# Optimization experiments

Measured on AMD Instinct MI355X. Metric: run time of the kernel, lower is better.

The kernel has to match this reference:

```python
import jax, jax.numpy as jnp
import numpy as np

NUM_USERS = 100000
NUM_BOOKS = 50000
HIDDEN = 128
USER_FEAT = 256
BOOK_FEAT = 256
E_PER_REL = 500000
NUM_LAYERS = 2


def setup_inputs() -> dict:
    key = jax.random.key(0)
    ks = jax.random.split(key, 10)
    user_x = jax.random.normal(ks[0], (NUM_USERS, USER_FEAT), dtype=jnp.float32)
    book_x = jax.random.normal(ks[1], (NUM_BOOKS, BOOK_FEAT), dtype=jnp.float32)
    user_W = jax.random.normal(ks[2], (HIDDEN, USER_FEAT), dtype=jnp.float32) * 0.05
    user_b = jax.random.normal(ks[3], (HIDDEN,), dtype=jnp.float32) * 0.05
    book_W = jax.random.normal(ks[4], (HIDDEN, BOOK_FEAT), dtype=jnp.float32) * 0.05
    book_b = jax.random.normal(ks[5], (HIDDEN,), dtype=jnp.float32) * 0.05
    # edge_index[0] = user indices, edge_index[1] = book indices
    rates_edge = jnp.stack([
        jax.random.randint(ks[6], (E_PER_REL,), 0, NUM_USERS),
        jax.random.randint(ks[7], (E_PER_REL,), 0, NUM_BOOKS)])
    implicit_edge = jnp.stack([
        jax.random.randint(ks[8], (E_PER_REL,), 0, NUM_USERS),
        jax.random.randint(ks[9], (E_PER_REL,), 0, NUM_BOOKS)])
    return {"user_x": user_x, "book_x": book_x, "user_W": user_W,
            "user_b": user_b, "book_W": book_W, "book_b": book_b,
            "rates_edge": rates_edge, "implicit_edge": implicit_edge}


def _lightgcn(user_x, book_x, user_W, user_b, book_W, book_b, rates_edge, implicit_edge):
    num_users = user_x.shape[0]
    num_nodes = num_users + book_x.shape[0]
    # input projections
    cu = user_x @ user_W.T + user_b  # [U, H]
    cb = book_x @ book_W.T + book_b  # [B, H]
    user_embeds = [cu]
    book_embeds = [cb]
    # build full directed edge list exactly as in the torch source
    all_edges = jnp.concatenate([rates_edge, implicit_edge], axis=1)  # [2, E]
    book_to_user = jnp.stack([all_edges[1] + num_users, all_edges[0]])
    full_edge = jnp.concatenate([all_edges, book_to_user], axis=1)  # [2, 2E]
    row, col = full_edge[0], full_edge[1]
    # symmetric degree normalization (edges fixed across layers)
    deg = jax.ops.segment_sum(jnp.ones(col.shape, dtype=cu.dtype), col,
                              num_segments=num_nodes)
    deg_inv_sqrt = jnp.where(deg > 0, jax.lax.rsqrt(jnp.maximum(deg, 1.0) * 0 + jnp.where(deg > 0, deg, 1.0)), 0.0)
    deg_inv_sqrt = jnp.where(deg > 0, jax.lax.rsqrt(jnp.where(deg > 0, deg, 1.0)), 0.0)
    norm = deg_inv_sqrt[row] * deg_inv_sqrt[col]  # [2E]
    for _ in range(NUM_LAYERS):
        x = jnp.concatenate([cu, cb], axis=0)  # [U+B, H]
        msg = x[row] * norm[:, None]           # gather + scale, [2E, H]
        out = jax.ops.segment_sum(msg, col, num_segments=num_nodes)  # scatter-add
        cu = out[:num_users]
        cb = out[num_users:]
        user_embeds.append(cu)
        book_embeds.append(cb)
    final_user = jnp.mean(jnp.stack(user_embeds), axis=0)
    final_book = jnp.mean(jnp.stack(book_embeds), axis=0)
    return final_user, final_book


def reference(user_x, book_x, user_W, user_b, book_W, book_b, rates_edge, implicit_edge):
    return _lightgcn(user_x, book_x, user_W, user_b, book_W, book_b,
                     rates_edge, implicit_edge)
```

## Files before the change

kernel.cpp:

```cpp
#include <hip/hip_runtime.h>

#define NUSERS 100000
#define NBOOKS 50000
#define HID 128
#define FEAT 256
#define EPR 500000
#define NEDGE (2 * EPR)

#define UBLK64 ((NUSERS + 63) / 64)
#define BBLK64 ((NBOOKS + 63) / 64)
#define GH_BLOCKS (UBLK64 + BBLK64)
#define FILL_B ((NEDGE + 255) / 256)
#define DIS_B ((NUSERS + 255) / 256)

typedef __attribute__((ext_vector_type(8))) short bf16x8;
typedef __attribute__((ext_vector_type(4))) float f32x4;

__device__ __forceinline__ unsigned short f2bf(float f) {
  union { float f; unsigned u; } v; v.f = f;
  unsigned r = v.u + 0x7FFFu + ((v.u >> 16) & 1u);
  return (unsigned short)(r >> 16);
}
__device__ __forceinline__ float bf2f(unsigned short h) {
  union { unsigned u; float f; } v; v.u = ((unsigned)h) << 16;
  return v.f;
}
__device__ __forceinline__ unsigned pk2bf(float lo, float hi) {
  unsigned r;
  asm("v_cvt_pk_bf16_f32 %0, %1, %2" : "=v"(r) : "v"(lo), "v"(hi));
  return r;
}

__global__ void cast_w(const float* __restrict__ w0, const float* __restrict__ w1,
                       unsigned short* __restrict__ o0, unsigned short* __restrict__ o1)
{
  int i = blockIdx.x * 256 + threadIdx.x;
  if (i < HID * FEAT) { o0[i] = f2bf(w0[i]); o1[i] = f2bf(w1[i]); }
}

__device__ __forceinline__ void decode_edge(const int* __restrict__ rates,
                                            const int* __restrict__ impl,
                                            int i, int& u, int& bk)
{
  if (i < EPR) { u = rates[i]; bk = rates[EPR + i]; }
  else { int j = i - EPR; u = impl[j]; bk = impl[EPR + j]; }
}

__global__ __launch_bounds__(256) void gemm_hist(
    const float* __restrict__ Xu, const float* __restrict__ Xb,
    const unsigned short* __restrict__ Wu, const unsigned short* __restrict__ Wb,
    const float* __restrict__ bu, const float* __restrict__ bb,
    unsigned short* __restrict__ cu0b, float* __restrict__ outb,
    float* __restrict__ outu,
    const int* __restrict__ rates, const int* __restrict__ impl,
    int* __restrict__ degu, int* __restrict__ cntb,
    int* __restrict__ relpos)
{
  __shared__ float Asb[64 * 256];
  const int bid = blockIdx.x;
  const int tid = threadIdx.x;

  const int e0 = bid * 512 + tid;
  const int e1 = e0 + 256;
  const bool v0 = e0 < NEDGE, v1 = e1 < NEDGE;
  int p0 = 0, p1 = 0;
  if (v0) {
    int u, bk;
    decode_edge(rates, impl, e0, u, bk);
    p0 = atomicAdd(&cntb[bk], 1);
    atomicAdd(&degu[u], 1);
  }
  if (v1) {
    int u, bk;
    decode_edge(rates, impl, e1, u, bk);
    p1 = atomicAdd(&cntb[bk], 1);
    atomicAdd(&degu[u], 1);
  }

  const bool isU = bid < UBLK64;
  const float* __restrict__ X = isU ? Xu : Xb;
  const unsigned short* __restrict__ W = isU ? Wu : Wb;
  const float* __restrict__ bias = isU ? bu : bb;
  const int M  = isU ? NUSERS : NBOOKS;
  const int bm = (isU ? bid : bid - UBLK64) * 64;

  const int lane = tid & 63;
  const int wv   = tid >> 6;
  const int l15  = lane & 15, l4 = lane >> 4;

#pragma unroll
  for (int rnd = 0; rnd < 16; ++rnd) {
    int o   = wv * 1024 + rnd * 64 + lane;
    int row = o >> 6;
    int pc  = o & 63;
    int lc  = pc ^ (row & 7);
    int gr  = bm + row; if (gr > M - 1) gr = M - 1;
    __builtin_amdgcn_global_load_lds(
        (const float*)&X[(size_t)gr * FEAT + lc * 4],
        &Asb[(size_t)(wv * 1024 + rnd * 64) * 4], 16, 0, 0);
  }
  __syncthreads();

  f32x4 acc[8];
#pragma unroll
  for (int ni = 0; ni < 8; ++ni) acc[ni] = (f32x4)0.f;

  const int arow = wv * 16 + l15;
  const int m7   = l15 & 7;
#pragma unroll
  for (int ks = 0; ks < 8; ++ks) {
    bf16x8 bfr[8];
#pragma unroll
    for (int ni = 0; ni < 8; ++ni)
      bfr[ni] = *reinterpret_cast<const bf16x8*>(
          &W[(size_t)(ni * 16 + l15) * FEAT + ks * 32 + l4 * 8]);

    int lc0 = ks * 8 + l4 * 2;
    f32x4 a0 = *reinterpret_cast<const f32x4*>(&Asb[arow * 256 + ((lc0    ) ^ m7) * 4]);
    f32x4 a1 = *reinterpret_cast<const f32x4*>(&Asb[arow * 256 + ((lc0 + 1) ^ m7) * 4]);
    union { unsigned u32[4]; bf16x8 v; } au;
    au.u32[0] = pk2bf(a0[0], a0[1]);
    au.u32[1] = pk2bf(a0[2], a0[3]);
    au.u32[2] = pk2bf(a1[0], a1[1]);
    au.u32[3] = pk2bf(a1[2], a1[3]);

#pragma unroll
    for (int ni = 0; ni < 8; ++ni)
      acc[ni] = __builtin_amdgcn_mfma_f32_16x16x32_bf16(au.v, bfr[ni], acc[ni], 0, 0, 0);
  }

#pragma unroll
  for (int ni = 0; ni < 8; ++ni) {
    int col = ni * 16 + l15;
    float bj = bias[col];
#pragma unroll
    for (int j = 0; j < 4; ++j) {
      int rr = bm + wv * 16 + l4 * 4 + j;
      if (rr < M) {
        float vv = acc[ni][j] + bj;
        if (isU) {
          cu0b[(size_t)rr * HID + col] = f2bf(vv);
          if (rr >= NBOOKS) outu[(size_t)rr * HID + col] = vv * (1.0f / 3.0f);
        } else {
          outb[(size_t)rr * HID + col] = vv * (1.0f / 3.0f);
        }
      }
    }
  }

  if (v0) relpos[e0] = p0;
  if (v1) relpos[e1] = p1;
}

__global__ void fill_dis(const int* __restrict__ rates, const int* __restrict__ impl,
                         const int* __restrict__ offs,
                         const int* __restrict__ relpos,
                         int* __restrict__ brow,
                         const int* __restrict__ degu, const int* __restrict__ cntb,
                         float* __restrict__ dis)
{
  int b = blockIdx.x;
  if (b >= FILL_B) {
    int i = (b - FILL_B) * 256 + threadIdx.x;
    if (i < NUSERS) {
      int d = degu[i] + (i < NBOOKS ? cntb[i] : 0);
      dis[i] = (d > 0) ? rsqrtf((float)d) : 0.f;
    }
    return;
  }
  int i = b * 256 + threadIdx.x;
  if (i >= NEDGE) return;
  int u, bk;
  decode_edge(rates, impl, i, u, bk);
  brow[offs[bk] + relpos[i]] = u;
}

__global__ __launch_bounds__(1024) void scan_blocks(const int* __restrict__ counts,
                                                    int* __restrict__ offs,
                                                    int* __restrict__ bsum, int N)
{
  __shared__ int buf[1024];
  int t = threadIdx.x;
  int i = blockIdx.x * 1024 + t;
  int v = (i < N) ? counts[i] : 0;
  buf[t] = v;
  __syncthreads();
  for (int off = 1; off < 1024; off <<= 1) {
    int x = (t >= off) ? buf[t - off] : 0;
    __syncthreads();
    buf[t] += x;
    __syncthreads();
  }
  int incl = buf[t];
  if (i < N) offs[i] = incl - v;
  if (t == 1023) bsum[blockIdx.x] = incl;
}

__global__ void scan_totals(const int* __restrict__ bsum, int* __restrict__ bpre,
                            int* __restrict__ offs, int nb, int N)
{
  if (threadIdx.x == 0 && blockIdx.x == 0) {
    int run = 0;
    for (int b = 0; b < nb; ++b) { bpre[b] = run; run += bsum[b]; }
    offs[N] = run;
  }
}

__global__ void add_prefix(int* __restrict__ offs, const int* __restrict__ bpre, int N)
{
  int i = blockIdx.x * blockDim.x + threadIdx.x;
  if (i < N) offs[i] += bpre[i >> 10];
}

__global__ __launch_bounds__(256) void pull1(const unsigned short* __restrict__ srcb,
    const int* __restrict__ offs, const int* __restrict__ brow,
    const float* __restrict__ dis, unsigned short* __restrict__ dstb)
{
  int c = (blockIdx.x << 2) + (threadIdx.x >> 6);
  if (c >= NBOOKS) return;
  const int lane = threadIdx.x & 63;
  const int g = lane >> 4, l = lane & 15;
  const int s = offs[c], e = offs[c + 1];

  float acc[8];
#pragma unroll
  for (int j = 0; j < 8; ++j) acc[j] = 0.f;

  int i = s + g;
  for (; i + 4 < e; i += 8) {
    int rr0 = brow[i], rr1 = brow[i + 4];
    float w0 = dis[rr0], w1 = dis[rr1];
    bf16x8 v0 = *reinterpret_cast<const bf16x8*>(&srcb[(size_t)rr0 * HID + l * 8]);
    bf16x8 v1 = *reinterpret_cast<const bf16x8*>(&srcb[(size_t)rr1 * HID + l * 8]);
#pragma unroll
    for (int j = 0; j < 8; ++j) acc[j] += w0 * bf2f((unsigned short)v0[j]);
#pragma unroll
    for (int j = 0; j < 8; ++j) acc[j] += w1 * bf2f((unsigned short)v1[j]);
  }
  if (i < e) {
    int rr = brow[i];
    float w = dis[rr];
    bf16x8 v = *reinterpret_cast<const bf16x8*>(&srcb[(size_t)rr * HID + l * 8]);
#pragma unroll
    for (int j = 0; j < 8; ++j) acc[j] += w * bf2f((unsigned short)v[j]);
  }

#pragma unroll
  for (int j = 0; j < 8; ++j) {
    acc[j] += __shfl_xor(acc[j], 16, 64);
    acc[j] += __shfl_xor(acc[j], 32, 64);
  }
  if (g == 0) {
    float db = dis[c];
    bf16x8 o;
#pragma unroll
    for (int j = 0; j < 8; ++j) o[j] = (short)f2bf(db * acc[j]);
    *reinterpret_cast<bf16x8*>(&dstb[(size_t)c * HID + l * 8]) = o;
  }
}

__global__ __launch_bounds__(256) void pull2_final(const unsigned short* __restrict__ h1b,
    const int* __restrict__ offs, const int* __restrict__ brow,
    const float* __restrict__ dis, const unsigned short* __restrict__ cu0b,
    float* __restrict__ outu)
{
  int c = (blockIdx.x << 2) + (threadIdx.x >> 6);
  if (c >= NBOOKS) return;
  const int lane = threadIdx.x & 63;
  const int g = lane >> 4, l = lane & 15;
  const int s = offs[c], e = offs[c + 1];

  float acc[8];
#pragma unroll
  for (int j = 0; j < 8; ++j) acc[j] = 0.f;

  int i = s + g;
  for (; i + 4 < e; i += 8) {
    int rr0 = brow[i], rr1 = brow[i + 4];
    int rc0 = rr0 < NBOOKS ? rr0 : 0;
    int rc1 = rr1 < NBOOKS ? rr1 : 0;
    float w0 = rr0 < NBOOKS ? dis[rr0] : 0.f;
    float w1 = rr1 < NBOOKS ? dis[rr1] : 0.f;
    bf16x8 v0 = *reinterpret_cast<const bf16x8*>(&h1b[(size_t)rc0 * HID + l * 8]);
    bf16x8 v1 = *reinterpret_cast<const bf16x8*>(&h1b[(size_t)rc1 * HID + l * 8]);
#pragma unroll
    for (int j = 0; j < 8; ++j) acc[j] += w0 * bf2f((unsigned short)v0[j]);
#pragma unroll
    for (int j = 0; j < 8; ++j) acc[j] += w1 * bf2f((unsigned short)v1[j]);
  }
  if (i < e) {
    int rr = brow[i];
    int rc = rr < NBOOKS ? rr : 0;
    float w = rr < NBOOKS ? dis[rr] : 0.f;
    bf16x8 v = *reinterpret_cast<const bf16x8*>(&h1b[(size_t)rc * HID + l * 8]);
#pragma unroll
    for (int j = 0; j < 8; ++j) acc[j] += w * bf2f((unsigned short)v[j]);
  }

#pragma unroll
  for (int j = 0; j < 8; ++j) {
    acc[j] += __shfl_xor(acc[j], 16, 64);
    acc[j] += __shfl_xor(acc[j], 32, 64);
  }
  if (g == 0) {
    float db = dis[c];
    size_t idx = (size_t)c * HID + l * 8;
    bf16x8 c0 = *reinterpret_cast<const bf16x8*>(&cu0b[idx]);
    bf16x8 h1 = *reinterpret_cast<const bf16x8*>(&h1b[idx]);
    float r[8];
#pragma unroll
    for (int j = 0; j < 8; ++j)
      r[j] = (bf2f((unsigned short)c0[j]) + bf2f((unsigned short)h1[j]) + db * acc[j]) * (1.0f / 3.0f);
    *reinterpret_cast<float4*>(&outu[idx])     = make_float4(r[0], r[1], r[2], r[3]);
    *reinterpret_cast<float4*>(&outu[idx + 4]) = make_float4(r[4], r[5], r[6], r[7]);
  }
}

extern "C" void kernel_launch(void* const* d_in, const int* in_sizes, int n_in,
                              void* d_out, int out_size, void* d_ws, size_t ws_size,
                              hipStream_t stream)
{
  const float* user_x = (const float*)d_in[0];
  const float* book_x = (const float*)d_in[1];
  const float* user_W = (const float*)d_in[2];
  const float* user_b = (const float*)d_in[3];
  const float* book_W = (const float*)d_in[4];
  const float* book_b = (const float*)d_in[5];
  const int*   rates  = (const int*)d_in[6];
  const int*   impl   = (const int*)d_in[7];

  float* out      = (float*)d_out;
  float* out_user = out;
  float* out_book = out + (size_t)NUSERS * HID;

  char* p = (char*)d_ws;
  auto carve = [&](size_t bytes) -> void* {
    void* r = (void*)p;
    p += (bytes + 255) & ~(size_t)255;
    return r;
  };
  unsigned short* cu0b   = (unsigned short*)carve((size_t)NUSERS * HID * 2);
  unsigned short* h1b    = (unsigned short*)carve((size_t)NBOOKS * HID * 2);
  unsigned short* wub    = (unsigned short*)carve((size_t)HID * FEAT * 2);
  unsigned short* wbb    = (unsigned short*)carve((size_t)HID * FEAT * 2);
  int*   degu   = (int*)carve((size_t)NUSERS * 4);
  int*   cntb   = (int*)carve((size_t)NBOOKS * 4);
  float* dis    = (float*)carve((size_t)NUSERS * 4);
  int*   offs   = (int*)carve((size_t)(NBOOKS + 2) * 4);
  int*   bsum   = (int*)carve(256 * 4);
  int*   bpre   = (int*)carve(256 * 4);
  int*   relpos = (int*)carve((size_t)NEDGE * 4);
  int*   brow   = (int*)carve((size_t)NEDGE * 4);

  hipMemsetAsync(degu, 0, (size_t)NUSERS * 4, stream);
  hipMemsetAsync(cntb, 0, (size_t)NBOOKS * 4, stream);

  cast_w<<<(HID * FEAT + 255) / 256, 256, 0, stream>>>(user_W, book_W, wub, wbb);

  gemm_hist<<<GH_BLOCKS, 256, 0, stream>>>(
      user_x, book_x, wub, wbb, user_b, book_b,
      cu0b, out_book, out_user, rates, impl, degu, cntb, relpos);

  const int nb = (NBOOKS + 1023) / 1024;
  scan_blocks<<<nb, 1024, 0, stream>>>(cntb, offs, bsum, NBOOKS);
  scan_totals<<<1, 64, 0, stream>>>(bsum, bpre, offs, nb, NBOOKS);
  add_prefix<<<(NBOOKS + 255) / 256, 256, 0, stream>>>(offs, bpre, NBOOKS);

  fill_dis<<<FILL_B + DIS_B, 256, 0, stream>>>(rates, impl, offs, relpos, brow,
                                               degu, cntb, dis);

  pull1<<<(NBOOKS + 3) / 4, 256, 0, stream>>>(cu0b, offs, brow, dis, h1b);
  pull2_final<<<(NBOOKS + 3) / 4, 256, 0, stream>>>(h1b, offs, brow, dis, cu0b, out_user);
}
```

Baseline: 278.5 us.

## Cut GEMM LDS footprint with per-wave half-K staging and move histogram atomics last

The projection GEMM now stages A through a per-wave 8KB LDS buffer, filled in two K-halves with an XOR swizzle. Each wave waits only on its own loads, so the block-wide __syncthreads and most of the previous 64KB shared allocation go away, which should raise occupancy. The edge histogram atomics and relpos writes now run after the GEMM epilogue instead of before it. The trade-off is that each half's global load is exposed per wave with no overlap against the MFMA work.

```diff
diff --git a/kernel.cpp b/kernel.cpp
--- a/kernel.cpp
+++ b/kernel.cpp
@@ -56,77 +56,70 @@
     int* __restrict__ degu, int* __restrict__ cntb,
     int* __restrict__ relpos)
 {
-  __shared__ float Asb[64 * 256];
+  __shared__ float Asb[4][2048];
   const int bid = blockIdx.x;
   const int tid = threadIdx.x;
-
-  const int e0 = bid * 512 + tid;
-  const int e1 = e0 + 256;
-  const bool v0 = e0 < NEDGE, v1 = e1 < NEDGE;
-  int p0 = 0, p1 = 0;
-  if (v0) {
-    int u, bk;
-    decode_edge(rates, impl, e0, u, bk);
-    p0 = atomicAdd(&cntb[bk], 1);
-    atomicAdd(&degu[u], 1);
-  }
-  if (v1) {
-    int u, bk;
-    decode_edge(rates, impl, e1, u, bk);
-    p1 = atomicAdd(&cntb[bk], 1);
-    atomicAdd(&degu[u], 1);
-  }
+  const int lane = tid & 63;
+  const int wv   = tid >> 6;
+  const int l15  = lane & 15, l4 = lane >> 4;
 
   const bool isU = bid < UBLK64;
   const float* __restrict__ X = isU ? Xu : Xb;
   const unsigned short* __restrict__ W = isU ? Wu : Wb;
   const float* __restrict__ bias = isU ? bu : bb;
-  const int M  = isU ? NUSERS : NBOOKS;
-  const int bm = (isU ? bid : bid - UBLK64) * 64;
-
-  const int lane = tid & 63;
-  const int wv   = tid >> 6;
-  const int l15  = lane & 15, l4 = lane >> 4;
-
-#pragma unroll
-  for (int rnd = 0; rnd < 16; ++rnd) {
-    int o   = wv * 1024 + rnd * 64 + lane;
-    int row = o >> 6;
-    int pc  = o & 63;
-    int lc  = pc ^ (row & 7);
-    int gr  = bm + row; if (gr > M - 1) gr = M - 1;
-    __builtin_amdgcn_global_load_lds(
-        (const float*)&X[(size_t)gr * FEAT + lc * 4],
-        &Asb[(size_t)(wv * 1024 + rnd * 64) * 4], 16, 0, 0);
-  }
-  __syncthreads();
+  const int M    = isU ? NUSERS : NBOOKS;
+  const int bm   = (isU ? bid : bid - UBLK64) * 64;
+  const int wrow = bm + wv * 16;
+
+  float* wbase = &Asb[wv][0];
 
   f32x4 acc[8];
 #pragma unroll
   for (int ni = 0; ni < 8; ++ni) acc[ni] = (f32x4)0.f;
 
-  const int arow = wv * 16 + l15;
-  const int m7   = l15 & 7;
-#pragma unroll
-  for (int ks = 0; ks < 8; ++ks) {
-    bf16x8 bfr[8];
-#pragma unroll
-    for (int ni = 0; ni < 8; ++ni)
-      bfr[ni] = *reinterpret_cast<const bf16x8*>(
-          &W[(size_t)(ni * 16 + l15) * FEAT + ks * 32 + l4 * 8]);
-
-    int lc0 = ks * 8 + l4 * 2;
-    f32x4 a0 = *reinterpret_cast<const f32x4*>(&Asb[arow * 256 + ((lc0    ) ^ m7) * 4]);
-    f32x4 a1 = *reinterpret_cast<const f32x4*>(&Asb[arow * 256 + ((lc0 + 1) ^ m7) * 4]);
-    union { unsigned u32[4]; bf16x8 v; } au;
-    au.u32[0] = pk2bf(a0[0], a0[1]);
-    au.u32[1] = pk2bf(a0[2], a0[3]);
-    au.u32[2] = pk2bf(a1[0], a1[1]);
-    au.u32[3] = pk2bf(a1[2], a1[3]);
-
-#pragma unroll
-    for (int ni = 0; ni < 8; ++ni)
-      acc[ni] = __builtin_amdgcn_mfma_f32_16x16x32_bf16(au.v, bfr[ni], acc[ni], 0, 0, 0);
+#pragma unroll
+  for (int h = 0; h < 2; ++h) {
+    if (h) {
+      asm volatile("s_waitcnt lgkmcnt(0)" ::: "memory");
+      __builtin_amdgcn_sched_barrier(0);
+    }
+#pragma unroll
+    for (int rnd = 0; rnd < 8; ++rnd) {
+      int o = rnd * 64 + lane;
+      int r = o >> 5;
+      int c = o & 31;
+      int lc = c ^ r;
+      int gr = wrow + r; if (gr > M - 1) gr = M - 1;
+      __builtin_amdgcn_global_load_lds(
+          (const float*)&X[(size_t)gr * FEAT + h * 128 + lc * 4],
+          wbase + rnd * 256, 16, 0, 0);
+    }
+    asm volatile("s_waitcnt vmcnt(0)" ::: "memory");
+    __builtin_amdgcn_sched_barrier(0);
+
+#pragma unroll
+    for (int ks = 0; ks < 4; ++ks) {
+      const int kg = h * 4 + ks;
+      bf16x8 bfr[8];
+#pragma unroll
+      for (int ni = 0; ni < 8; ++ni)
+        bfr[ni] = *reinterpret_cast<const bf16x8*>(
+            &W[(size_t)(ni * 16 + l15) * FEAT + kg * 32 + l4 * 8]);
+
+      int u0 = (ks * 8 + l4 * 2) ^ l15;
+      int u1 = (ks * 8 + l4 * 2 + 1) ^ l15;
+      f32x4 a0 = *reinterpret_cast<const f32x4*>(&wbase[(l15 * 32 + u0) * 4]);
+      f32x4 a1 = *reinterpret_cast<const f32x4*>(&wbase[(l15 * 32 + u1) * 4]);
+      union { unsigned u32[4]; bf16x8 v; } au;
+      au.u32[0] = pk2bf(a0[0], a0[1]);
+      au.u32[1] = pk2bf(a0[2], a0[3]);
+      au.u32[2] = pk2bf(a1[0], a1[1]);
+      au.u32[3] = pk2bf(a1[2], a1[3]);
+
+#pragma unroll
+      for (int ni = 0; ni < 8; ++ni)
+        acc[ni] = __builtin_amdgcn_mfma_f32_16x16x32_bf16(au.v, bfr[ni], acc[ni], 0, 0, 0);
+    }
   }
 
 #pragma unroll
@@ -135,7 +128,7 @@
     float bj = bias[col];
 #pragma unroll
     for (int j = 0; j < 4; ++j) {
-      int rr = bm + wv * 16 + l4 * 4 + j;
+      int rr = wrow + l4 * 4 + j;
       if (rr < M) {
         float vv = acc[ni][j] + bj;
         if (isU) {
@@ -148,8 +141,22 @@
     }
   }
 
-  if (v0) relpos[e0] = p0;
-  if (v1) relpos[e1] = p1;
+  const int e0 = bid * 512 + tid;
+  const int e1 = e0 + 256;
+  if (e0 < NEDGE) {
+    int u, bk;
+    decode_edge(rates, impl, e0, u, bk);
+    int p0 = atomicAdd(&cntb[bk], 1);
+    atomicAdd(&degu[u], 1);
+    relpos[e0] = p0;
+  }
+  if (e1 < NEDGE) {
+    int u, bk;
+    decode_edge(rates, impl, e1, u, bk);
+    int p1 = atomicAdd(&cntb[bk], 1);
+    atomicAdd(&degu[u], 1);
+    relpos[e1] = p1;
+  }
 }
 
 __global__ void fill_dis(const int* __restrict__ rates, const int* __restrict__ impl,
```

Result: no change. 275.5 us (-1.1%).
